# Performance work log

Hardware: AMD Instinct MI355X
Metric: run time of the kernel (lower is better)

The kernel has to match this reference:

```python
import jax, jax.numpy as jnp
import numpy as np

N, IN_DIM, H, D = 4096, 512, 8, 64
NEG = -1e9  # additive mask value for non-edges


def setup_inputs() -> dict:
    key = jax.random.key(0)
    k1, k2, k3, k4, k5, k6 = jax.random.split(key, 6)
    data = jax.random.normal(k1, (N, IN_DIM), dtype=jnp.float32)
    r = jax.random.uniform(k2, (N, N), dtype=jnp.float32)
    connectivity = jnp.where(r < 0.05, 0.0, NEG).astype(jnp.float32)
    # xavier-uniform-ish init for params
    lim_w = float(np.sqrt(6.0 / (IN_DIM + H * D)))
    W = jax.random.uniform(k3, (H * D, IN_DIM), jnp.float32, -lim_w, lim_w)
    b = jnp.zeros((H * D,), jnp.float32)
    lim_p = float(np.sqrt(6.0 / (H * D + 1)))
    src_proj = jax.random.uniform(k4, (1, H, D), jnp.float32, -lim_p, lim_p)
    trg_proj = jax.random.uniform(k5, (1, H, D), jnp.float32, -lim_p, lim_p)
    return {"data": data, "connectivity": connectivity, "W": W, "b": b,
            "src_proj": src_proj, "trg_proj": trg_proj}


def reference(data, connectivity, W, b, src_proj, trg_proj):
    # dropout is identity in eval mode (reference is deterministic)
    data1 = (data @ W.T + b).reshape(N, H, D)          # (N,H,D)
    src = jnp.einsum('nhd,xhd->nh', data1, src_proj)   # (N,H)
    trg = jnp.einsum('nhd,xhd->nh', data1, trg_proj)   # (N,H)
    # scores: (H,N,1) + (H,1,N) broadcast outer-sum
    e = src.T[:, :, None] + trg.T[:, None, :]          # (H,N,N)
    e = jnp.where(e >= 0, e, 0.01 * e)                 # LeakyReLU(0.01)
    e = e + connectivity[None, :, :]                   # additive mask
    scores = jax.nn.softmax(e, axis=-1)                # (H,N,N)
    # bmm over heads: (H,N,N) x (H,N,D) -> (H,N,D)
    out = jnp.einsum('hnm,hmd->hnd', scores, data1.transpose(1, 0, 2))
    out = out.transpose(1, 0, 2).reshape(N, H * D)     # concat=True
    return out
```

## Files before the change

### kernel.cpp

```cpp
#include <hip/hip_runtime.h>
#include <hip/hip_bf16.h>

#define NN 4096
#define IN_DIM 512
#define NH 8
#define DD 64
#define HD 512
#define QCAP 128
#define RCAP 448


typedef __attribute__((ext_vector_type(8))) short short8;
typedef __attribute__((ext_vector_type(4))) float f32x4;
typedef __attribute__((ext_vector_type(2))) float f32x2;

#define LOG2E 1.4426950408889634f

static __device__ __forceinline__ unsigned short f2bf(float x) {
    __hip_bfloat16 h = __float2bfloat16(x);
    return *reinterpret_cast<unsigned short*>(&h);
}

static __device__ __forceinline__ f32x2 bf2f(unsigned u) {
    __hip_bfloat162 b = *reinterpret_cast<const __hip_bfloat162*>(&u);
    float2 f = __bfloat1622float2(b);
    f32x2 r = {f.x, f.y};
    return r;
}

__global__ __launch_bounds__(256) void k_cast2(const float* __restrict__ inA,
                                               unsigned short* __restrict__ outA,
                                               int n4A,
                                               const float* __restrict__ inB,
                                               unsigned short* __restrict__ outB,
                                               int n4B) {
    int t = blockIdx.x * 256 + threadIdx.x;
    const float* in;
    unsigned short* out;
    if (t < n4A) {
        in = inA; out = outA;
    } else {
        t -= n4A;
        if (t >= n4B) return;
        in = inB; out = outB;
    }
    float4 v = ((const float4*)in)[t];
    ushort4 o;
    o.x = f2bf(v.x); o.y = f2bf(v.y); o.z = f2bf(v.z); o.w = f2bf(v.w);
    ((ushort4*)out)[t] = o;
}

__global__ __launch_bounds__(256) void k_gemm_fused(const unsigned short* __restrict__ Ab,
                                                    const unsigned short* __restrict__ Wb,
                                                    const float* __restrict__ bias,
                                                    const float* __restrict__ sp,
                                                    const float* __restrict__ tp,
                                                    unsigned short* __restrict__ Cb,
                                                    float* __restrict__ src,
                                                    float* __restrict__ trg) {
    const int lane = threadIdx.x & 63;
    const int w = threadIdx.x >> 6;
    const int col = lane & 15;
    const int quad = lane >> 4;
    const int koff = quad * 8;
    const int h = blockIdx.x;
    const int m0 = h * 64;
    const int n0 = blockIdx.y * 64;

    const short8* ap  = (const short8*)(Ab + (size_t)(n0 + w * 16 + col) * IN_DIM + koff);
    const short8* bp0 = (const short8*)(Wb + (size_t)(m0 +  0 + col) * IN_DIM + koff);
    const short8* bp1 = (const short8*)(Wb + (size_t)(m0 + 16 + col) * IN_DIM + koff);
    const short8* bp2 = (const short8*)(Wb + (size_t)(m0 + 32 + col) * IN_DIM + koff);
    const short8* bp3 = (const short8*)(Wb + (size_t)(m0 + 48 + col) * IN_DIM + koff);

    f32x4 acc0 = {0.f, 0.f, 0.f, 0.f}, acc1 = acc0, acc2 = acc0, acc3 = acc0;

#pragma unroll 4
    for (int ks = 0; ks < 16; ks++) {
        short8 a  = ap[ks * 4];
        short8 b0 = bp0[ks * 4];
        short8 b1 = bp1[ks * 4];
        short8 b2 = bp2[ks * 4];
        short8 b3 = bp3[ks * 4];
        acc0 = __builtin_amdgcn_mfma_f32_16x16x32_bf16(a, b0, acc0, 0, 0, 0);
        acc1 = __builtin_amdgcn_mfma_f32_16x16x32_bf16(a, b1, acc1, 0, 0, 0);
        acc2 = __builtin_amdgcn_mfma_f32_16x16x32_bf16(a, b2, acc2, 0, 0, 0);
        acc3 = __builtin_amdgcn_mfma_f32_16x16x32_bf16(a, b3, acc3, 0, 0, 0);
    }

    const int rbase = n0 + w * 16 + quad * 4;
    f32x4 accs[4] = {acc0, acc1, acc2, acc3};
    float ps[4] = {0.f, 0.f, 0.f, 0.f};
    float pt[4] = {0.f, 0.f, 0.f, 0.f};
#pragma unroll
    for (int mt = 0; mt < 4; mt++) {
        const int m = m0 + mt * 16 + col;
        const float bv  = bias[m];
        const float spv = sp[m];
        const float tpv = tp[m];
#pragma unroll
        for (int r = 0; r < 4; r++) {
            float v = accs[mt][r] + bv;
            Cb[(size_t)(rbase + r) * HD + m] = f2bf(v);
            ps[r] += v * spv;
            pt[r] += v * tpv;
        }
    }
#pragma unroll
    for (int off = 1; off <= 8; off <<= 1) {
#pragma unroll
        for (int r = 0; r < 4; r++) {
            ps[r] += __shfl_xor(ps[r], off, 64);
            pt[r] += __shfl_xor(pt[r], off, 64);
        }
    }
    if (col < 4)
        src[(rbase + col) * 8 + h] = ps[col] * LOG2E;
    else if (col < 8)
        trg[(rbase + col - 4) * 8 + h] = pt[col - 4] * LOG2E;
}

__global__ __launch_bounds__(256) void k_rowattn(const float* __restrict__ conn,
                                                 const float* __restrict__ src,
                                                 const float* __restrict__ trg,
                                                 const unsigned short* __restrict__ d1b,
                                                 float* __restrict__ out,
                                                 int rowbase) {
    __shared__ unsigned short seg[4][QCAP];
    __shared__ unsigned short elist[RCAP + 8];
    __shared__ int wcnt[4];
    __shared__ float cbuf[3][32][17];
    const int w = threadIdx.x >> 6, lane = threadIdx.x & 63;
    const int i = rowbase + blockIdx.x;

    const float* crow = conn + (size_t)i * NN + w * 1024;
    int cnt = 0;
#pragma unroll
    for (int c0 = 0; c0 < 1024; c0 += 256) {
        float4 c = *(const float4*)(crow + c0 + lane * 4);
        float cv[4] = {c.x, c.y, c.z, c.w};
#pragma unroll
        for (int q = 0; q < 4; q++) {
            bool edge = (cv[q] == 0.0f);
            unsigned long long mask = __ballot(edge);
            int pre = __popcll(mask & ((1ull << lane) - 1ull));
            int pos = cnt + pre;
            if (edge && pos < QCAP)
                seg[w][pos] = (unsigned short)(w * 1024 + c0 + lane * 4 + q);
            cnt += __popcll(mask);
        }
    }
    if (cnt > QCAP) cnt = QCAP;
    if (lane == 0) wcnt[w] = cnt;
    __syncthreads();

    const int c0n = wcnt[0], c1n = wcnt[1], c2n = wcnt[2], c3n = wcnt[3];
    int tot = c0n + c1n + c2n + c3n;
    if (tot > RCAP) tot = RCAP;
    const int base = (w == 0) ? 0 : (w == 1) ? c0n
                   : (w == 2) ? c0n + c1n : c0n + c1n + c2n;
    for (int k = lane; k < cnt && base + k < RCAP; k += 64)
        elist[base + k] = seg[w][k];
    __syncthreads();
    if (threadIdx.x < 8)
        elist[tot + threadIdx.x] = (tot > 0) ? elist[tot - 1] : (unsigned short)0;
    __syncthreads();

    const int e = lane >> 5;
    const int l32 = lane & 31;
    const int h = l32 >> 2;
    const int d4 = l32 & 3;
    const float sh = src[i * 8 + h];
    const unsigned voffB = (unsigned)(h * 128 + d4 * 32);
    const unsigned char* vb = (const unsigned char*)d1b;
    const int kbeg = (tot * w) >> 2;
    const int kend = (tot * (w + 1)) >> 2;
    const int np = (kend - kbeg + 1) >> 1;

    f32x2 a0 = {0.f, 0.f}, a1 = a0, a2 = a0, a3 = a0,
          a4 = a0, a5 = a0, a6 = a0, a7 = a0;
    float lsum = 0.f;
    if (np > 0) {
        int myk = kbeg + e;
        unsigned j0 = elist[myk];
        unsigned j1 = elist[myk + 2];
        unsigned j2 = elist[myk + 4];
        float t0 = trg[j0 * 8 + h];
        float t1 = trg[j1 * 8 + h];
        float t2 = trg[j2 * 8 + h];
        uint4 U0a = *(const uint4*)(vb + (j0 << 10) + voffB);
        uint4 U0b = *(const uint4*)(vb + (j0 << 10) + voffB + 16);
        uint4 U1a = *(const uint4*)(vb + (j1 << 10) + voffB);
        uint4 U1b = *(const uint4*)(vb + (j1 << 10) + voffB + 16);
        uint4 U2a = *(const uint4*)(vb + (j2 << 10) + voffB);
        uint4 U2b = *(const uint4*)(vb + (j2 << 10) + voffB + 16);
#pragma unroll 3
        for (int kp = 0; kp < np; kp++) {
            unsigned j3 = elist[myk + 6];
            float t3 = trg[j3 * 8 + h];
            uint4 U3a = *(const uint4*)(vb + (j3 << 10) + voffB);
            uint4 U3b = *(const uint4*)(vb + (j3 << 10) + voffB + 16);
            float ev = sh + t0;
            ev = fmaxf(ev, 0.01f * ev);
            float p = (myk < kend) ? exp2f(ev) : 0.f;
            lsum += p;
            f32x2 p2 = {p, p};
            a0 += p2 * bf2f(U0a.x);
            a1 += p2 * bf2f(U0a.y);
            a2 += p2 * bf2f(U0a.z);
            a3 += p2 * bf2f(U0a.w);
            a4 += p2 * bf2f(U0b.x);
            a5 += p2 * bf2f(U0b.y);
            a6 += p2 * bf2f(U0b.z);
            a7 += p2 * bf2f(U0b.w);
            t0 = t1; t1 = t2; t2 = t3;
            U0a = U1a; U0b = U1b;
            U1a = U2a; U1b = U2b;
            U2a = U3a; U2b = U3b;
            myk += 2;
        }
    }

    float acc[16] = {a0.x, a0.y, a1.x, a1.y, a2.x, a2.y, a3.x, a3.y,
                     a4.x, a4.y, a5.x, a5.y, a6.x, a6.y, a7.x, a7.y};
#pragma unroll
    for (int r = 0; r < 16; r++) acc[r] += __shfl_xor(acc[r], 32, 64);
    lsum += __shfl_xor(lsum, 32, 64);

    if (w > 0 && e == 0) {
#pragma unroll
        for (int r = 0; r < 16; r++) cbuf[w - 1][l32][r] = acc[r];
        cbuf[w - 1][l32][16] = lsum;
    }
    __syncthreads();
    if (w == 0 && e == 0) {
#pragma unroll
        for (int wv = 0; wv < 3; wv++) {
#pragma unroll
            for (int r = 0; r < 16; r++) acc[r] += cbuf[wv][l32][r];
            lsum += cbuf[wv][l32][16];
        }
        float inv = (lsum > 0.f) ? (1.f / lsum) : 0.f;
        float* op = out + (size_t)i * HD + h * 64 + d4 * 16;
#pragma unroll
        for (int q = 0; q < 4; q++)
            *(float4*)(op + q * 4) = make_float4(acc[q * 4 + 0] * inv, acc[q * 4 + 1] * inv,
                                                 acc[q * 4 + 2] * inv, acc[q * 4 + 3] * inv);
    }
}

extern "C" void kernel_launch(void* const* d_in, const int* in_sizes, int n_in,
                              void* d_out, int out_size, void* d_ws, size_t ws_size,
                              hipStream_t stream) {
    const float* data = (const float*)d_in[0];
    const float* conn = (const float*)d_in[1];
    const float* W    = (const float*)d_in[2];
    const float* bias = (const float*)d_in[3];
    const float* sp   = (const float*)d_in[4];
    const float* tp   = (const float*)d_in[5];
    float* out = (float*)d_out;

    unsigned short* d1b = (unsigned short*)d_ws;
    unsigned short* Ab  = d1b + (size_t)NN * HD;
    unsigned short* Wb  = Ab + (size_t)NN * IN_DIM;
    float* src  = (float*)(Wb + (size_t)HD * IN_DIM);
    float* trg  = src + NN * NH;

    const int n4A = NN * IN_DIM / 4;
    const int n4B = HD * IN_DIM / 4;
    k_cast2<<<dim3((n4A + n4B + 255) / 256), 256, 0, stream>>>(data, Ab, n4A, W, Wb, n4B);
    k_gemm_fused<<<dim3(NH, NN / 64), 256, 0, stream>>>(Ab, Wb, bias, sp, tp, d1b, src, trg);
    k_rowattn<<<dim3(NN / 2), 256, 0, stream>>>(conn, src, trg, d1b, out, 0);
    k_rowattn<<<dim3(NN / 2), 256, 0, stream>>>(conn, src, trg, d1b, out, NN / 2);
}
```

Before: 174.8 us.

## Split GEMM tiles across waves, prefetch K-loads, and merge row-attention launches

The projection GEMM now uses 32-row by 64-column tiles per block. Each wave computes a 16x32 sub-tile, so the grid has twice as many blocks. The per-head src/trg partial dot products from the two column halves are combined through shared memory and a barrier. The K loop software-prefetches the next A/B fragments into registers. The two half-size row-attention launches are merged into a single launch of NN blocks to cut launch overhead, at the cost of more redundant A-fragment loads per block and an extra sync.

```diff
diff --git a/kernel.cpp b/kernel.cpp
--- a/kernel.cpp
+++ b/kernel.cpp
@@ -58,42 +58,45 @@
                                                     unsigned short* __restrict__ Cb,
                                                     float* __restrict__ src,
                                                     float* __restrict__ trg) {
+    __shared__ float sbuf[32][2];
     const int lane = threadIdx.x & 63;
     const int w = threadIdx.x >> 6;
+    const int rhalf = w & 1;
+    const int mhalf = w >> 1;
     const int col = lane & 15;
     const int quad = lane >> 4;
     const int koff = quad * 8;
     const int h = blockIdx.x;
-    const int m0 = h * 64;
-    const int n0 = blockIdx.y * 64;
-
-    const short8* ap  = (const short8*)(Ab + (size_t)(n0 + w * 16 + col) * IN_DIM + koff);
+    const int m0 = h * 64 + mhalf * 32;
+    const int n0 = blockIdx.y * 32;
+
+    const short8* ap  = (const short8*)(Ab + (size_t)(n0 + rhalf * 16 + col) * IN_DIM + koff);
     const short8* bp0 = (const short8*)(Wb + (size_t)(m0 +  0 + col) * IN_DIM + koff);
     const short8* bp1 = (const short8*)(Wb + (size_t)(m0 + 16 + col) * IN_DIM + koff);
-    const short8* bp2 = (const short8*)(Wb + (size_t)(m0 + 32 + col) * IN_DIM + koff);
-    const short8* bp3 = (const short8*)(Wb + (size_t)(m0 + 48 + col) * IN_DIM + koff);
-
-    f32x4 acc0 = {0.f, 0.f, 0.f, 0.f}, acc1 = acc0, acc2 = acc0, acc3 = acc0;
-
+
+    f32x4 acc0 = {0.f, 0.f, 0.f, 0.f}, acc1 = acc0;
+
+    short8 a  = ap[0];
+    short8 b0 = bp0[0];
+    short8 b1 = bp1[0];
 #pragma unroll 4
     for (int ks = 0; ks < 16; ks++) {
-        short8 a  = ap[ks * 4];
-        short8 b0 = bp0[ks * 4];
-        short8 b1 = bp1[ks * 4];
-        short8 b2 = bp2[ks * 4];
-        short8 b3 = bp3[ks * 4];
+        const int kn = (ks + 1 < 16) ? (ks + 1) * 4 : 15 * 4;
+        short8 an  = ap[kn];
+        short8 b0n = bp0[kn];
+        short8 b1n = bp1[kn];
         acc0 = __builtin_amdgcn_mfma_f32_16x16x32_bf16(a, b0, acc0, 0, 0, 0);
         acc1 = __builtin_amdgcn_mfma_f32_16x16x32_bf16(a, b1, acc1, 0, 0, 0);
-        acc2 = __builtin_amdgcn_mfma_f32_16x16x32_bf16(a, b2, acc2, 0, 0, 0);
-        acc3 = __builtin_amdgcn_mfma_f32_16x16x32_bf16(a, b3, acc3, 0, 0, 0);
-    }
-
-    const int rbase = n0 + w * 16 + quad * 4;
-    f32x4 accs[4] = {acc0, acc1, acc2, acc3};
+        a = an; b0 = b0n; b1 = b1n;
+    }
+
+    const int rbase = n0 + rhalf * 16 + quad * 4;
+    const int row_local = rhalf * 16 + quad * 4;
+    f32x4 accs[2] = {acc0, acc1};
     float ps[4] = {0.f, 0.f, 0.f, 0.f};
     float pt[4] = {0.f, 0.f, 0.f, 0.f};
 #pragma unroll
-    for (int mt = 0; mt < 4; mt++) {
+    for (int mt = 0; mt < 2; mt++) {
         const int m = m0 + mt * 16 + col;
         const float bv  = bias[m];
         const float spv = sp[m];
@@ -114,24 +117,30 @@
             pt[r] += __shfl_xor(pt[r], off, 64);
         }
     }
-    if (col < 4)
-        src[(rbase + col) * 8 + h] = ps[col] * LOG2E;
-    else if (col < 8)
-        trg[(rbase + col - 4) * 8 + h] = pt[col - 4] * LOG2E;
+    if (mhalf == 1) {
+        if (col < 4) sbuf[row_local + col][0] = ps[col];
+        else if (col < 8) sbuf[row_local + col - 4][1] = pt[col - 4];
+    }
+    __syncthreads();
+    if (mhalf == 0) {
+        if (col < 4)
+            src[(rbase + col) * 8 + h] = (ps[col] + sbuf[row_local + col][0]) * LOG2E;
+        else if (col < 8)
+            trg[(rbase + col - 4) * 8 + h] = (pt[col - 4] + sbuf[row_local + col - 4][1]) * LOG2E;
+    }
 }
 
 __global__ __launch_bounds__(256) void k_rowattn(const float* __restrict__ conn,
                                                  const float* __restrict__ src,
                                                  const float* __restrict__ trg,
                                                  const unsigned short* __restrict__ d1b,
-                                                 float* __restrict__ out,
-                                                 int rowbase) {
+                                                 float* __restrict__ out) {
     __shared__ unsigned short seg[4][QCAP];
     __shared__ unsigned short elist[RCAP + 8];
     __shared__ int wcnt[4];
     __shared__ float cbuf[3][32][17];
     const int w = threadIdx.x >> 6, lane = threadIdx.x & 63;
-    const int i = rowbase + blockIdx.x;
+    const int i = blockIdx.x;
 
     const float* crow = conn + (size_t)i * NN + w * 1024;
     int cnt = 0;
@@ -269,7 +278,6 @@
     const int n4A = NN * IN_DIM / 4;
     const int n4B = HD * IN_DIM / 4;
     k_cast2<<<dim3((n4A + n4B + 255) / 256), 256, 0, stream>>>(data, Ab, n4A, W, Wb, n4B);
-    k_gemm_fused<<<dim3(NH, NN / 64), 256, 0, stream>>>(Ab, Wb, bias, sp, tp, d1b, src, trg);
-    k_rowattn<<<dim3(NN / 2), 256, 0, stream>>>(conn, src, trg, d1b, out, 0);
-    k_rowattn<<<dim3(NN / 2), 256, 0, stream>>>(conn, src, trg, d1b, out, NN / 2);
-}
+    k_gemm_fused<<<dim3(NH, NN / 32), 256, 0, stream>>>(Ab, Wb, bias, sp, tp, d1b, src, trg);
+    k_rowattn<<<dim3(NN), 256, 0, stream>>>(conn, src, trg, d1b, out);
+}
```

After: 176.4 us. Within noise of the previous version (+1.0%).
